# Kernel tuning notes

Hardware: AMD Instinct MI355X
Metric: run time of the kernel (lower is better)

The kernel has to match this reference:

```python
import jax, jax.numpy as jnp
import numpy as np

ALPHA = 0.2  # LeakyReLU negative slope
NEG_INF = -9e15


def setup_inputs() -> dict:
    key = jax.random.key(0)
    ks = jax.random.split(key, 9)
    B, N, Fin, Fout, H = 4, 1024, 256, 256, 32
    h = jax.random.normal(ks[0], (B, N, Fin), dtype=jnp.float32)
    mz = jax.random.uniform(ks[1], (B, N, 1), dtype=jnp.float32) * 2000.0
    adj = jax.random.randint(ks[2], (B, N, N), 0, 2, dtype=jnp.int32)
    # xavier_uniform with gain=1.414
    def xavier(k, shape, gain=1.414):
        fan_in, fan_out = shape[0], shape[1]
        bound = gain * np.sqrt(6.0 / (fan_in + fan_out))
        return jax.random.uniform(k, shape, jnp.float32, -bound, bound)
    W = xavier(ks[3], (Fin, Fout))
    a = xavier(ks[4], (2 * Fout, 1))
    w1 = xavier(ks[5], (1, H), gain=1.0)
    b1 = jnp.zeros((H,), jnp.float32)
    w2 = xavier(ks[6], (H, 1), gain=1.0)
    b2 = jnp.zeros((1,), jnp.float32)
    return {"h": h, "mz": mz, "W": W, "a": a, "w1": w1, "b1": b1, "w2": w2, "b2": b2, "adj": adj}


def reference(h, mz, W, a, w1, b1, w2, b2, adj):
    # h: (B,N,Fin), mz: (B,N,1), adj: (B,N,N)
    Wh = jnp.matmul(h, W)                       # (B,N,Fout)
    Fout = W.shape[1]
    a1 = a[:Fout, 0]                            # (Fout,)
    a2 = a[Fout:, 0]                            # (Fout,)
    # e[b,i,j] = leaky_relu(Wh[b,i]@a1 + Wh[b,j]@a2)  (identical to concat trick)
    s1 = jnp.einsum('bnf,f->bn', Wh, a1)
    s2 = jnp.einsum('bnf,f->bn', Wh, a2)
    e = jax.nn.leaky_relu(s1[:, :, None] + s2[:, None, :], negative_slope=ALPHA)  # (B,N,N)
    # |mz_i - mz_j| with first row/col zeroed
    diff = jnp.abs(mz - jnp.swapaxes(mz, 1, 2))  # (B,N,N)
    diff = diff.at[:, 0, :].set(0.0)
    diff = diff.at[:, :, 0].set(0.0)
    # tiny per-edge MLP: Linear(1,32)->ReLU->Linear(32,1)
    hdn = jax.nn.relu(diff[..., None] * w1[0] + b1)       # (B,N,N,32)
    diff_term = jnp.einsum('bijh,h->bij', hdn, w2[:, 0]) + b2[0]
    e = e + diff_term
    att = jnp.where(adj > 0, e, NEG_INF)
    att = jax.nn.softmax(att, axis=2)
    # dropout is identity in eval mode
    h_prime = jnp.matmul(att, Wh)               # (B,N,Fout)
    return jax.nn.elu(h_prime)
```

## Files before the change

### kernel.cpp

```cpp
#include <hip/hip_runtime.h>
#include <hip/hip_bf16.h>

#define ALPHA 0.2f
#define NEGINF -9000000000000000.0f

typedef __attribute__((ext_vector_type(8))) short short8;
typedef __attribute__((ext_vector_type(4))) float f32x4;
typedef __attribute__((ext_vector_type(4))) int i32x4;
typedef __attribute__((ext_vector_type(4))) unsigned short u16x4;

static constexpr int NB = 4, NN = 1024, NF = 256, NH = 32;

__device__ __forceinline__ unsigned short f2bf(float x) {
  union { float f; unsigned u; } v; v.f = x;
  unsigned r = v.u + 0x7fffu + ((v.u >> 16) & 1u);
  return (unsigned short)(r >> 16);
}

__global__ __launch_bounds__(256) void prep_kernel(
    const float* __restrict__ W, const float* __restrict__ a,
    float* __restrict__ wa1, float* __restrict__ wa2,
    unsigned short* __restrict__ WTp) {
  int k = blockIdx.x;
  int t = threadIdx.x;
  float w = W[k * NF + t];
  WTp[(((k >> 3) * NF) + t) * 8 + (k & 7)] = f2bf(w);
  float p1 = w * a[t];
  float p2 = w * a[NF + t];
#pragma unroll
  for (int off = 32; off >= 1; off >>= 1) {
    p1 += __shfl_xor(p1, off);
    p2 += __shfl_xor(p2, off);
  }
  __shared__ float r1[4], r2[4];
  if ((t & 63) == 0) { r1[t >> 6] = p1; r2[t >> 6] = p2; }
  __syncthreads();
  if (t == 0) {
    wa1[k] = r1[0] + r1[1] + r1[2] + r1[3];
    wa2[k] = r2[0] + r2[1] + r2[2] + r2[3];
  }
}

__global__ __launch_bounds__(512) void wh_kernel(
    const float* __restrict__ h, const unsigned short* __restrict__ WTp,
    const float* __restrict__ wa1, const float* __restrict__ wa2,
    unsigned short* __restrict__ WhP, float* __restrict__ s1g,
    float* __restrict__ s2g) {
  __shared__ unsigned short hs[16 * 256];
  int bid = blockIdx.x;
  int b = bid >> 6;
  int rb = (bid & 63) << 4;
  int t = threadIdx.x;
  {
    int row = t >> 5, c0 = (t & 31) * 8;
    const float* src = h + (size_t)(b * NN + rb + row) * NF + c0;
    f32x4 v0 = *(const f32x4*)src;
    f32x4 v1 = *(const f32x4*)(src + 4);
    unsigned short tmp[8] = {f2bf(v0.x), f2bf(v0.y), f2bf(v0.z), f2bf(v0.w),
                             f2bf(v1.x), f2bf(v1.y), f2bf(v1.z), f2bf(v1.w)};
    int off = row * 512 + ((c0 * 2) ^ ((row & 7) << 4));
    *(short8*)((char*)hs + off) = *(const short8*)tmp;
    f32x4 a10 = *(const f32x4*)(wa1 + c0);
    f32x4 a11 = *(const f32x4*)(wa1 + c0 + 4);
    f32x4 a20 = *(const f32x4*)(wa2 + c0);
    f32x4 a21 = *(const f32x4*)(wa2 + c0 + 4);
    float d1 = v0.x * a10.x + v0.y * a10.y + v0.z * a10.z + v0.w * a10.w +
               v1.x * a11.x + v1.y * a11.y + v1.z * a11.z + v1.w * a11.w;
    float d2 = v0.x * a20.x + v0.y * a20.y + v0.z * a20.z + v0.w * a20.w +
               v1.x * a21.x + v1.y * a21.y + v1.z * a21.z + v1.w * a21.w;
#pragma unroll
    for (int off2 = 16; off2 >= 1; off2 >>= 1) {
      d1 += __shfl_xor(d1, off2);
      d2 += __shfl_xor(d2, off2);
    }
    if ((t & 31) == 0) {
      s1g[b * NN + rb + row] = d1;
      s2g[b * NN + rb + row] = d2;
    }
  }
  __syncthreads();
  int wid = t >> 6, lane = t & 63;
  int fb = wid * 32;
  int rowa = lane & 15, kg = lane >> 4;
  f32x4 acc0 = {0.f, 0.f, 0.f, 0.f}, acc1 = {0.f, 0.f, 0.f, 0.f};
#pragma unroll
  for (int ks = 0; ks < 8; ++ks) {
    int k0 = ks * 32;
    short8 af = *(const short8*)((const char*)hs + rowa * 512 +
                                 ((2 * (k0 + kg * 8)) ^ ((rowa & 7) << 4)));
    int kc = ks * 4 + kg;
    short8 bf0 = *(const short8*)(WTp + ((kc * NF) + fb + (lane & 15)) * 8);
    short8 bf1 = *(const short8*)(WTp + ((kc * NF) + fb + 16 + (lane & 15)) * 8);
    acc0 = __builtin_amdgcn_mfma_f32_16x16x32_bf16(af, bf0, acc0, 0, 0, 0);
    acc1 = __builtin_amdgcn_mfma_f32_16x16x32_bf16(af, bf1, acc1, 0, 0, 0);
  }
#pragma unroll
  for (int r = 0; r < 4; ++r) {
    int jl = (lane >> 4) * 4 + r;
    int j = rb + jl;
    int base = ((b << 7) + (j >> 3)) * NF;
    WhP[(size_t)(base + fb + (lane & 15)) * 8 + (j & 7)] = f2bf(acc0[r]);
    WhP[(size_t)(base + fb + 16 + (lane & 15)) * 8 + (j & 7)] = f2bf(acc1[r]);
  }
}

__global__ __launch_bounds__(1024) void attn_kernel(
    const float* __restrict__ mz, const int* __restrict__ adj,
    const unsigned short* __restrict__ WhP,
    const float* __restrict__ w1, const float* __restrict__ b1,
    const float* __restrict__ w2, const float* __restrict__ b2,
    const float* __restrict__ s1g, const float* __restrict__ s2g,
    float* __restrict__ out) {
  __shared__ unsigned short Pb[32 * 1024];
  __shared__ float mzs[1024];
  __shared__ float s2s[1024];
  __shared__ float s1s[32];
  __shared__ float rinv[32];
  __shared__ float segsh[3];

  int bid0 = blockIdx.x;
  int bid = (bid0 & 7) * 16 + (bid0 >> 3);
  int b = bid >> 5;
  int rb = (bid & 31) << 5;
  int t = threadIdx.x;
  int wid = t >> 6, lane = t & 63;

  i32x4 adjreg[8];
  {
    const int* adjb = adj + (size_t)b * NN * NN;
#pragma unroll
    for (int rr = 0; rr < 2; ++rr) {
      int ig = rb + wid * 2 + rr;
#pragma unroll
      for (int c = 0; c < 4; ++c)
        adjreg[rr * 4 + c] =
            *(const i32x4*)(adjb + (size_t)ig * NN + c * 256 + lane * 4);
    }
  }

  if (t < NH) {
    float w1h = w1[t], b1h = b1[t], w2h = w2[t];
    bool bp = (w1h != 0.f) && (b1h != 0.f) && ((b1h > 0.f) != (w1h > 0.f));
    bool act = (w1h + b1h) > 0.f;
    float cA = act ? w2h * w1h : 0.f;
    float cB = act ? w2h * b1h : 0.f;
    float nbp = bp ? 1.f : 0.f;
#pragma unroll
    for (int off = 16; off >= 1; off >>= 1) {
      cA += __shfl_xor(cA, off);
      cB += __shfl_xor(cB, off);
      nbp += __shfl_xor(nbp, off);
    }
    if (t == 0) {
      segsh[0] = (nbp == 0.f) ? 1.f : 0.f;
      segsh[1] = cA;
      segsh[2] = cB + b2[0];
    }
  }
  mzs[t] = mz[b * NN + t];
  s2s[t] = s2g[b * NN + t];
  if (t < 32) s1s[t] = s1g[b * NN + rb + t];
  __syncthreads();

  float segF = segsh[0], segA = segsh[1], segB = segsh[2];
  float b2v = b2[0];
  for (int rr = 0; rr < 2; ++rr) {
    int row = wid * 2 + rr;
    int ig = rb + row;
    float s1v = s1s[row];
    float mzi = mzs[ig];
    float e[16];
    if (segF != 0.f) {
#pragma unroll
      for (int c = 0; c < 4; ++c) {
        int j0 = c * 256 + lane * 4;
        i32x4 av = adjreg[rr * 4 + c];
        f32x4 mzv = *(const f32x4*)(mzs + j0);
        f32x4 s2v = *(const f32x4*)(s2s + j0);
#pragma unroll
        for (int u = 0; u < 4; ++u) {
          float dd = fabsf(mzi - mzv[u]);
          float d = (ig == 0 || (j0 + u) == 0) ? 0.f : dd;
          float s = s1v + s2v[u];
          s = fmaxf(s, 0.f) + ALPHA * fminf(s, 0.f);
          float ee = s + fmaf(d, segA, segB);
          e[c * 4 + u] = (av[u] > 0) ? ee : NEGINF;
        }
      }
    } else {
#pragma unroll
      for (int c = 0; c < 4; ++c) {
        int j0 = c * 256 + lane * 4;
        i32x4 av = adjreg[rr * 4 + c];
        f32x4 mzv = *(const f32x4*)(mzs + j0);
        f32x4 s2v = *(const f32x4*)(s2s + j0);
        float d[4], acc[4];
#pragma unroll
        for (int u = 0; u < 4; ++u) {
          float dd = fabsf(mzi - mzv[u]);
          d[u] = (ig == 0 || (j0 + u) == 0) ? 0.f : dd;
          acc[u] = b2v;
        }
#pragma unroll 1
        for (int hh = 0; hh < NH; ++hh) {
          float w1h = w1[hh], b1h = b1[hh], w2h = w2[hh];
#pragma unroll
          for (int u = 0; u < 4; ++u)
            acc[u] += fmaxf(d[u] * w1h + b1h, 0.f) * w2h;
        }
#pragma unroll
        for (int u = 0; u < 4; ++u) {
          float s = s1v + s2v[u];
          s = s > 0.f ? s : ALPHA * s;
          e[c * 4 + u] = (av[u] > 0) ? (s + acc[u]) : NEGINF;
        }
      }
    }
    float m = -3.0e38f;
#pragma unroll
    for (int q = 0; q < 16; ++q) m = fmaxf(m, e[q]);
#pragma unroll
    for (int off = 32; off >= 1; off >>= 1) m = fmaxf(m, __shfl_xor(m, off));
    float sum = 0.f;
#pragma unroll
    for (int q = 0; q < 16; ++q) {
      e[q] = __expf(e[q] - m);
      sum += e[q];
    }
#pragma unroll
    for (int off = 32; off >= 1; off >>= 1) sum += __shfl_xor(sum, off);
#pragma unroll
    for (int c = 0; c < 4; ++c) {
      u16x4 pk = {f2bf(e[c * 4 + 0]), f2bf(e[c * 4 + 1]),
                  f2bf(e[c * 4 + 2]), f2bf(e[c * 4 + 3])};
      int byteoff = row * 2048 + ((512 * c + 8 * lane) ^ ((row & 7) << 4));
      *(u16x4*)((char*)Pb + byteoff) = pk;
    }
    if (lane == 0) rinv[row] = 1.0f / sum;
  }
  __syncthreads();

  {
    int fb = wid * 16;
    int fl = lane & 15, kg = lane >> 4;
    const unsigned short* whb = WhP + (((size_t)b) << 7) * NF * 8;
    f32x4 acc0 = {0.f, 0.f, 0.f, 0.f}, acc1 = {0.f, 0.f, 0.f, 0.f};
    int abase = fl * 2048;
#pragma unroll 4
    for (int ks = 0; ks < 32; ++ks) {
      int k0 = ks * 32;
      int kc = ks * 4 + kg;
      short8 bf = *(const short8*)(whb + (size_t)((kc * NF) + fb + fl) * 8);
      int aoff = (2 * (k0 + kg * 8)) ^ ((fl & 7) << 4);
      short8 af0 = *(const short8*)((const char*)Pb + abase + aoff);
      short8 af1 = *(const short8*)((const char*)Pb + abase + 32768 + aoff);
      acc0 = __builtin_amdgcn_mfma_f32_16x16x32_bf16(af0, bf, acc0, 0, 0, 0);
      acc1 = __builtin_amdgcn_mfma_f32_16x16x32_bf16(af1, bf, acc1, 0, 0, 0);
    }
#pragma unroll
    for (int r = 0; r < 4; ++r) {
      int il0 = (lane >> 4) * 4 + r;
      int il1 = il0 + 16;
      float x0 = acc0[r] * rinv[il0];
      float x1 = acc1[r] * rinv[il1];
      x0 = x0 > 0.f ? x0 : (__expf(x0) - 1.f);
      x1 = x1 > 0.f ? x1 : (__expf(x1) - 1.f);
      out[(size_t)(b * NN + rb + il0) * NF + fb + fl] = x0;
      out[(size_t)(b * NN + rb + il1) * NF + fb + fl] = x1;
    }
  }
}

extern "C" void kernel_launch(void* const* d_in, const int* in_sizes, int n_in,
                              void* d_out, int out_size, void* d_ws, size_t ws_size,
                              hipStream_t stream) {
  const float* h   = (const float*)d_in[0];
  const float* mz  = (const float*)d_in[1];
  const float* W   = (const float*)d_in[2];
  const float* a   = (const float*)d_in[3];
  const float* w1  = (const float*)d_in[4];
  const float* b1  = (const float*)d_in[5];
  const float* w2  = (const float*)d_in[6];
  const float* b2  = (const float*)d_in[7];
  const int*   adj = (const int*)d_in[8];
  float* out = (float*)d_out;

  unsigned short* WTp = (unsigned short*)d_ws;
  unsigned short* WhP = WTp + 65536;
  float* wa1 = (float*)(WhP + (size_t)NB * NN * NF);
  float* wa2 = wa1 + 256;
  float* s1g = wa2 + 256;
  float* s2g = s1g + NB * NN;

  prep_kernel<<<dim3(256), dim3(256), 0, stream>>>(W, a, wa1, wa2, WTp);
  wh_kernel<<<dim3(256), dim3(512), 0, stream>>>(h, WTp, wa1, wa2, WhP, s1g, s2g);
  attn_kernel<<<dim3(128), dim3(1024), 0, stream>>>(mz, adj, WhP, w1, b1, w2,
                                                    b2, s1g, s2g, out);
}
```

Baseline: 27.38 us.

## Pack adjacency into bitmasks in wh_kernel and read bits in attn_kernel

```diff
diff --git a/kernel.cpp b/kernel.cpp
--- a/kernel.cpp
+++ b/kernel.cpp
@@ -6,7 +6,6 @@
 
 typedef __attribute__((ext_vector_type(8))) short short8;
 typedef __attribute__((ext_vector_type(4))) float f32x4;
-typedef __attribute__((ext_vector_type(4))) int i32x4;
 typedef __attribute__((ext_vector_type(4))) unsigned short u16x4;
 
 static constexpr int NB = 4, NN = 1024, NF = 256, NH = 32;
@@ -44,13 +43,26 @@
 __global__ __launch_bounds__(512) void wh_kernel(
     const float* __restrict__ h, const unsigned short* __restrict__ WTp,
     const float* __restrict__ wa1, const float* __restrict__ wa2,
-    unsigned short* __restrict__ WhP, float* __restrict__ s1g,
-    float* __restrict__ s2g) {
+    const int* __restrict__ adj, unsigned short* __restrict__ WhP,
+    float* __restrict__ s1g, float* __restrict__ s2g,
+    unsigned long long* __restrict__ adjm) {
   __shared__ unsigned short hs[16 * 256];
   int bid = blockIdx.x;
   int b = bid >> 6;
   int rb = (bid & 63) << 4;
   int t = threadIdx.x;
+  int wid = t >> 6, lane = t & 63;
+
+  int av[32];
+  {
+    const int* adjb = adj + ((size_t)(b * NN + rb)) * NN;
+#pragma unroll
+    for (int i = 0; i < 32; ++i) {
+      int p = wid * 32 + i;
+      av[i] = adjb[(size_t)(p >> 4) * NN + (p & 15) * 64 + lane];
+    }
+  }
+
   {
     int row = t >> 5, c0 = (t & 31) * 8;
     const float* src = h + (size_t)(b * NN + rb + row) * NF + c0;
@@ -79,39 +91,51 @@
     }
   }
   __syncthreads();
-  int wid = t >> 6, lane = t & 63;
-  int fb = wid * 32;
-  int rowa = lane & 15, kg = lane >> 4;
-  f32x4 acc0 = {0.f, 0.f, 0.f, 0.f}, acc1 = {0.f, 0.f, 0.f, 0.f};
-#pragma unroll
-  for (int ks = 0; ks < 8; ++ks) {
-    int k0 = ks * 32;
-    short8 af = *(const short8*)((const char*)hs + rowa * 512 +
-                                 ((2 * (k0 + kg * 8)) ^ ((rowa & 7) << 4)));
-    int kc = ks * 4 + kg;
-    short8 bf0 = *(const short8*)(WTp + ((kc * NF) + fb + (lane & 15)) * 8);
-    short8 bf1 = *(const short8*)(WTp + ((kc * NF) + fb + 16 + (lane & 15)) * 8);
-    acc0 = __builtin_amdgcn_mfma_f32_16x16x32_bf16(af, bf0, acc0, 0, 0, 0);
-    acc1 = __builtin_amdgcn_mfma_f32_16x16x32_bf16(af, bf1, acc1, 0, 0, 0);
-  }
-#pragma unroll
-  for (int r = 0; r < 4; ++r) {
-    int jl = (lane >> 4) * 4 + r;
-    int j = rb + jl;
-    int base = ((b << 7) + (j >> 3)) * NF;
-    WhP[(size_t)(base + fb + (lane & 15)) * 8 + (j & 7)] = f2bf(acc0[r]);
-    WhP[(size_t)(base + fb + 16 + (lane & 15)) * 8 + (j & 7)] = f2bf(acc1[r]);
+  {
+    int fb = wid * 32;
+    int rowa = lane & 15, kg = lane >> 4;
+    f32x4 acc0 = {0.f, 0.f, 0.f, 0.f}, acc1 = {0.f, 0.f, 0.f, 0.f};
+#pragma unroll
+    for (int ks = 0; ks < 8; ++ks) {
+      int k0 = ks * 32;
+      short8 af = *(const short8*)((const char*)hs + rowa * 512 +
+                                   ((2 * (k0 + kg * 8)) ^ ((rowa & 7) << 4)));
+      int kc = ks * 4 + kg;
+      short8 bf0 = *(const short8*)(WTp + ((kc * NF) + fb + (lane & 15)) * 8);
+      short8 bf1 = *(const short8*)(WTp + ((kc * NF) + fb + 16 + (lane & 15)) * 8);
+      acc0 = __builtin_amdgcn_mfma_f32_16x16x32_bf16(af, bf0, acc0, 0, 0, 0);
+      acc1 = __builtin_amdgcn_mfma_f32_16x16x32_bf16(af, bf1, acc1, 0, 0, 0);
+    }
+#pragma unroll
+    for (int r = 0; r < 4; ++r) {
+      int jl = (lane >> 4) * 4 + r;
+      int j = rb + jl;
+      int base = ((b << 7) + (j >> 3)) * NF;
+      WhP[(size_t)(base + fb + (lane & 15)) * 8 + (j & 7)] = f2bf(acc0[r]);
+      WhP[(size_t)(base + fb + 16 + (lane & 15)) * 8 + (j & 7)] = f2bf(acc1[r]);
+    }
+  }
+
+  {
+#pragma unroll
+    for (int i = 0; i < 32; ++i) {
+      unsigned long long m = __ballot(av[i] > 0);
+      int p = wid * 32 + i;
+      if (lane == 0)
+        adjm[(size_t)(b * NN + rb + (p >> 4)) * 16 + (p & 15)] = m;
+    }
   }
 }
 
 __global__ __launch_bounds__(1024) void attn_kernel(
-    const float* __restrict__ mz, const int* __restrict__ adj,
+    const float* __restrict__ mz, const unsigned long long* __restrict__ adjm,
     const unsigned short* __restrict__ WhP,
     const float* __restrict__ w1, const float* __restrict__ b1,
     const float* __restrict__ w2, const float* __restrict__ b2,
     const float* __restrict__ s1g, const float* __restrict__ s2g,
     float* __restrict__ out) {
   __shared__ unsigned short Pb[32 * 1024];
+  __shared__ unsigned long long adjmsh[32][16];
   __shared__ float mzs[1024];
   __shared__ float s2s[1024];
   __shared__ float s1s[32];
@@ -125,19 +149,10 @@
   int t = threadIdx.x;
   int wid = t >> 6, lane = t & 63;
 
-  i32x4 adjreg[8];
-  {
-    const int* adjb = adj + (size_t)b * NN * NN;
-#pragma unroll
-    for (int rr = 0; rr < 2; ++rr) {
-      int ig = rb + wid * 2 + rr;
-#pragma unroll
-      for (int c = 0; c < 4; ++c)
-        adjreg[rr * 4 + c] =
-            *(const i32x4*)(adjb + (size_t)ig * NN + c * 256 + lane * 4);
-    }
-  }
-
+  if (t < 512) {
+    int r = t >> 4, sg = t & 15;
+    adjmsh[r][sg] = adjm[(size_t)(b * NN + rb + r) * 16 + sg];
+  }
   if (t < NH) {
     float w1h = w1[t], b1h = b1[t], w2h = w2[t];
     bool bp = (w1h != 0.f) && (b1h != 0.f) && ((b1h > 0.f) != (w1h > 0.f));
@@ -174,7 +189,9 @@
 #pragma unroll
       for (int c = 0; c < 4; ++c) {
         int j0 = c * 256 + lane * 4;
-        i32x4 av = adjreg[rr * 4 + c];
+        unsigned nib =
+            (unsigned)(adjmsh[row][c * 4 + (lane >> 4)] >> ((lane & 15) * 4)) &
+            0xFu;
         f32x4 mzv = *(const f32x4*)(mzs + j0);
         f32x4 s2v = *(const f32x4*)(s2s + j0);
 #pragma unroll
@@ -184,14 +201,16 @@
           float s = s1v + s2v[u];
           s = fmaxf(s, 0.f) + ALPHA * fminf(s, 0.f);
           float ee = s + fmaf(d, segA, segB);
-          e[c * 4 + u] = (av[u] > 0) ? ee : NEGINF;
+          e[c * 4 + u] = (nib & (1u << u)) ? ee : NEGINF;
         }
       }
     } else {
 #pragma unroll
       for (int c = 0; c < 4; ++c) {
         int j0 = c * 256 + lane * 4;
-        i32x4 av = adjreg[rr * 4 + c];
+        unsigned nib =
+            (unsigned)(adjmsh[row][c * 4 + (lane >> 4)] >> ((lane & 15) * 4)) &
+            0xFu;
         f32x4 mzv = *(const f32x4*)(mzs + j0);
         f32x4 s2v = *(const f32x4*)(s2s + j0);
         float d[4], acc[4];
@@ -212,7 +231,7 @@
         for (int u = 0; u < 4; ++u) {
           float s = s1v + s2v[u];
           s = s > 0.f ? s : ALPHA * s;
-          e[c * 4 + u] = (av[u] > 0) ? (s + acc[u]) : NEGINF;
+          e[c * 4 + u] = (nib & (1u << u)) ? (s + acc[u]) : NEGINF;
         }
       }
     }
@@ -246,7 +265,7 @@
     const unsigned short* whb = WhP + (((size_t)b) << 7) * NF * 8;
     f32x4 acc0 = {0.f, 0.f, 0.f, 0.f}, acc1 = {0.f, 0.f, 0.f, 0.f};
     int abase = fl * 2048;
-#pragma unroll 4
+#pragma unroll 8
     for (int ks = 0; ks < 32; ++ks) {
       int k0 = ks * 32;
       int kc = ks * 4 + kg;
@@ -291,9 +310,11 @@
   float* wa2 = wa1 + 256;
   float* s1g = wa2 + 256;
   float* s2g = s1g + NB * NN;
+  unsigned long long* adjm = (unsigned long long*)(s2g + NB * NN);
 
   prep_kernel<<<dim3(256), dim3(256), 0, stream>>>(W, a, wa1, wa2, WTp);
-  wh_kernel<<<dim3(256), dim3(512), 0, stream>>>(h, WTp, wa1, wa2, WhP, s1g, s2g);
-  attn_kernel<<<dim3(128), dim3(1024), 0, stream>>>(mz, adj, WhP, w1, b1, w2,
+  wh_kernel<<<dim3(256), dim3(512), 0, stream>>>(h, WTp, wa1, wa2, adj, WhP,
+                                                 s1g, s2g, adjm);
+  attn_kernel<<<dim3(128), dim3(1024), 0, stream>>>(mz, adjm, WhP, w1, b1, w2,
                                                     b2, s1g, s2g, out);
 }
```

Measured after the change: 35.59 us. 1.3x slower.
